# Kernel tuning notes

Measured on AMD Instinct MI355X. Metric: run time of the kernel, lower is better.

## Reference

```python
import jax, jax.numpy as jnp
import numpy as np

NUM_FIELDS = 64
# itertools.combinations(range(n), 2) order == row-major upper-triangle (k=1)
_IU, _JU = np.triu_indices(NUM_FIELDS, k=1)
_IU = jnp.asarray(_IU)
_JU = jnp.asarray(_JU)


def setup_inputs() -> dict:
    key = jax.random.key(0)
    inputs = jax.random.normal(key, (16384, NUM_FIELDS, 32), dtype=jnp.float32)
    return {"inputs": inputs}


def reference(inputs) -> jnp.ndarray:
    # Gram matrix of field embeddings per sample: [B, F, F]
    gram = jnp.einsum("bfd,bgd->bfg", inputs, inputs)
    # Upper-triangle (i<j) pairs, same order as itertools.combinations: [B, F*(F-1)/2]
    return gram[:, _IU, _JU]
```

## Files before the change

### kernel.cpp

```cpp
#include <hip/hip_runtime.h>

#define NF 64
#define ND 32
#define NPAIR 2016
#define KSTR 40
#define SAMP_BF (NF * KSTR)

typedef __attribute__((ext_vector_type(8))) short bf16x8;
typedef __attribute__((ext_vector_type(4))) float f32x4;

__global__ __launch_bounds__(256, 4) void ip_gram_mfma(
    const float* __restrict__ in, float* __restrict__ out) {

    __shared__ unsigned short sh[4 * 2 * SAMP_BF];

    const int t = threadIdx.x;
    const int w = t >> 6;
    const int l = t & 63;
    const int s = blockIdx.x * 4 + w;

    unsigned short* __restrict__ xhi = sh + w * 2 * SAMP_BF;
    unsigned short* __restrict__ xlo = xhi + SAMP_BF;

    const float* src = in + (size_t)s * (NF * ND);

    #pragma unroll
    for (int it = 0; it < 8; ++it) {
        int idx4 = l + (it << 6);
        float4 v = ((const float4*)src)[idx4];
        int f  = idx4 >> 3;
        int k0 = (idx4 & 7) << 2;
        float xv[4] = {v.x, v.y, v.z, v.w};
        ushort4 hv, lv;
        unsigned short* hp = (unsigned short*)&hv;
        unsigned short* lp = (unsigned short*)&lv;
        #pragma unroll
        for (int e = 0; e < 4; ++e) {
            unsigned xb = __builtin_bit_cast(unsigned, xv[e]);
            hp[e] = (unsigned short)(xb >> 16);
            float hf = __builtin_bit_cast(float, xb & 0xFFFF0000u);
            float lf = xv[e] - hf;
            lp[e] = (unsigned short)(__builtin_bit_cast(unsigned, lf) >> 16);
        }
        *(ushort4*)&xhi[f * KSTR + k0] = hv;
        *(ushort4*)&xlo[f * KSTR + k0] = lv;
    }

    const int q = l >> 4;
    const int m = l & 15;
    bf16x8 fhi[4], flo[4];
    #pragma unroll
    for (int r = 0; r < 4; ++r) {
        int off = (r * 16 + m) * KSTR + (q << 3);
        fhi[r] = *(const bf16x8*)&xhi[off];
        flo[r] = *(const bf16x8*)&xlo[off];
    }

    float* dst = out + (size_t)s * NPAIR;
    #pragma unroll
    for (int ti = 0; ti < 4; ++ti) {
        #pragma unroll
        for (int tj = ti; tj < 4; ++tj) {
            f32x4 c = {0.f, 0.f, 0.f, 0.f};
            c = __builtin_amdgcn_mfma_f32_16x16x32_bf16(fhi[ti], fhi[tj], c, 0, 0, 0);
            c = __builtin_amdgcn_mfma_f32_16x16x32_bf16(fhi[ti], flo[tj], c, 0, 0, 0);
            c = __builtin_amdgcn_mfma_f32_16x16x32_bf16(flo[ti], fhi[tj], c, 0, 0, 0);
            int j = tj * 16 + m;
            #pragma unroll
            for (int r = 0; r < 4; ++r) {
                int i = ti * 16 + (q << 2) + r;
                if (ti < tj || j > i) {
                    int p = ((i * (127 - i)) >> 1) + j - i - 1;
                    dst[p] = c[r];
                }
            }
        }
    }
}

extern "C" void kernel_launch(void* const* d_in, const int* in_sizes, int n_in,
                              void* d_out, int out_size, void* d_ws, size_t ws_size,
                              hipStream_t stream) {
    const float* in = (const float*)d_in[0];
    float* out = (float*)d_out;
    const int nsamples = in_sizes[0] / (NF * ND);
    ip_gram_mfma<<<nsamples / 4, 256, 0, stream>>>(in, out);
}
```

Before: 232.8 us.

## Load MFMA fragments directly from global memory, drop LDS staging

Each lane now reads its two float4s per row straight from global memory in MFMA fragment layout and splits them into bf16 hi/lo in registers, which removes the shared-memory staging buffer and its write/read round trip. With no LDS in use, launch bounds are raised to allow 8 blocks per CU for more occupancy. Output stores become nontemporal to avoid polluting the cache. The global loads are less coalesced (32-byte chunks per lane spread across rows), which may cost some load efficiency.

```diff
diff --git a/kernel.cpp b/kernel.cpp
--- a/kernel.cpp
+++ b/kernel.cpp
@@ -3,57 +3,38 @@
 #define NF 64
 #define ND 32
 #define NPAIR 2016
-#define KSTR 40
-#define SAMP_BF (NF * KSTR)
 
 typedef __attribute__((ext_vector_type(8))) short bf16x8;
 typedef __attribute__((ext_vector_type(4))) float f32x4;
 
-__global__ __launch_bounds__(256, 4) void ip_gram_mfma(
+__global__ __launch_bounds__(256, 8) void ip_gram_mfma(
     const float* __restrict__ in, float* __restrict__ out) {
-
-    __shared__ unsigned short sh[4 * 2 * SAMP_BF];
 
     const int t = threadIdx.x;
     const int w = t >> 6;
     const int l = t & 63;
     const int s = blockIdx.x * 4 + w;
 
-    unsigned short* __restrict__ xhi = sh + w * 2 * SAMP_BF;
-    unsigned short* __restrict__ xlo = xhi + SAMP_BF;
-
-    const float* src = in + (size_t)s * (NF * ND);
-
-    #pragma unroll
-    for (int it = 0; it < 8; ++it) {
-        int idx4 = l + (it << 6);
-        float4 v = ((const float4*)src)[idx4];
-        int f  = idx4 >> 3;
-        int k0 = (idx4 & 7) << 2;
-        float xv[4] = {v.x, v.y, v.z, v.w};
-        ushort4 hv, lv;
-        unsigned short* hp = (unsigned short*)&hv;
-        unsigned short* lp = (unsigned short*)&lv;
-        #pragma unroll
-        for (int e = 0; e < 4; ++e) {
-            unsigned xb = __builtin_bit_cast(unsigned, xv[e]);
-            hp[e] = (unsigned short)(xb >> 16);
-            float hf = __builtin_bit_cast(float, xb & 0xFFFF0000u);
-            float lf = xv[e] - hf;
-            lp[e] = (unsigned short)(__builtin_bit_cast(unsigned, lf) >> 16);
-        }
-        *(ushort4*)&xhi[f * KSTR + k0] = hv;
-        *(ushort4*)&xlo[f * KSTR + k0] = lv;
-    }
-
     const int q = l >> 4;
     const int m = l & 15;
+
+    const float* src = in + (size_t)s * (NF * ND) + (q << 3);
+
     bf16x8 fhi[4], flo[4];
     #pragma unroll
     for (int r = 0; r < 4; ++r) {
-        int off = (r * 16 + m) * KSTR + (q << 3);
-        fhi[r] = *(const bf16x8*)&xhi[off];
-        flo[r] = *(const bf16x8*)&xlo[off];
+        const float* rowp = src + (r * 16 + m) * ND;
+        float4 v0 = ((const float4*)rowp)[0];
+        float4 v1 = ((const float4*)rowp)[1];
+        float xv[8] = {v0.x, v0.y, v0.z, v0.w, v1.x, v1.y, v1.z, v1.w};
+        #pragma unroll
+        for (int e = 0; e < 8; ++e) {
+            unsigned xb = __builtin_bit_cast(unsigned, xv[e]);
+            fhi[r][e] = (short)(xb >> 16);
+            float hf = __builtin_bit_cast(float, xb & 0xFFFF0000u);
+            float lf = xv[e] - hf;
+            flo[r][e] = (short)(__builtin_bit_cast(unsigned, lf) >> 16);
+        }
     }
 
     float* dst = out + (size_t)s * NPAIR;
@@ -71,7 +52,7 @@
                 int i = ti * 16 + (q << 2) + r;
                 if (ti < tj || j > i) {
                     int p = ((i * (127 - i)) >> 1) + j - i - 1;
-                    dst[p] = c[r];
+                    __builtin_nontemporal_store(c[r], &dst[p]);
                 }
             }
         }
```

New measurement: 325.1 us. 39.7% more time.
